# Kernel tuning notes

Hardware: AMD Instinct MI355X
Metric: run time of the kernel (lower is better)

The kernel has to match this reference:

```python
import jax, jax.numpy as jnp
import numpy as np

F, LP, NL, DG = 65536, 8, 8192, 64
D = 32  # path_state_dim == link_state_dim
ITERS = 8
MS = {'flow_traffic': (0.5, 2.0), 'flow_length': (0.5, 2.0), 'flow_loss_packet': (0.1, 5.0),
      'flow_propag_delay': (0.2, 3.0), 'link_capacity': (1.0, 1.0)}


def gru_cell(h, x, w, u, b):
    # Keras GRUCell (reset_after=True); gate order z, r, h
    mx = x @ w + b[0]
    mh = h @ u + b[1]
    xz, xr, xh = jnp.split(mx, 3, axis=-1)
    hz, hr, hh = jnp.split(mh, 3, axis=-1)
    z = jax.nn.sigmoid(xz + hz)
    r = jax.nn.sigmoid(xr + hr)
    c = jnp.tanh(xh + r * hh)
    return z * h + (1.0 - z) * c


def setup_inputs() -> dict:
    key = jax.random.key(0)
    ks = jax.random.split(key, 24)
    g = lambda i, shape: jax.random.normal(ks[i], shape, jnp.float32) * 0.1
    return dict(
        flow_traffic=jax.random.uniform(ks[0], (F, 1), jnp.float32),
        flow_length=jax.random.uniform(ks[1], (F, 1), jnp.float32),
        flow_loss_packet=jax.random.uniform(ks[2], (F, 1), jnp.float32),
        flow_propag_delay=jax.random.uniform(ks[3], (F, 1), jnp.float32),
        flow_packet_size=jax.random.uniform(ks[4], (F, 1), jnp.float32),
        link_capacity=jax.random.uniform(ks[5], (NL, 1), jnp.float32) + 0.5,
        link_to_flow=jax.random.randint(ks[6], (F, LP), 0, NL),
        flow_to_link_flow=jax.random.randint(ks[7], (NL, DG), 0, F),
        flow_to_link_pos=jax.random.randint(ks[8], (NL, DG), 0, LP + 1),
        fe_w1=g(9, (4, D)), fe_b1=jnp.zeros(D), fe_w2=g(10, (D, D)), fe_b2=jnp.zeros(D),
        le_w1=g(11, (2, D)), le_b1=jnp.zeros(D), le_w2=g(12, (D, D)), le_b2=jnp.zeros(D),
        att_w=g(13, (D, D)), att_b=jnp.zeros(D),
        pg_w=g(14, (D, 3 * D)), pg_u=g(15, (D, 3 * D)), pg_b=jnp.zeros((2, 3 * D)),
        lg_w=g(16, (D, 3 * D)), lg_u=g(17, (D, 3 * D)), lg_b=jnp.zeros((2, 3 * D)),
        ro_w1=g(18, (D, D // 2)), ro_b1=jnp.zeros(D // 2),
        ro_w2=g(19, (D // 2, D // 4)), ro_b2=jnp.zeros(D // 4),
        ro_w3=g(20, (D // 4, 1)), ro_b3=jnp.zeros(1),
    )


def reference(flow_traffic, flow_length, flow_loss_packet, flow_propag_delay, flow_packet_size,
              link_capacity, link_to_flow, flow_to_link_flow, flow_to_link_pos,
              fe_w1, fe_b1, fe_w2, fe_b2, le_w1, le_b1, le_w2, le_b2, att_w, att_b,
              pg_w, pg_u, pg_b, lg_w, lg_u, lg_b, ro_w1, ro_b1, ro_w2, ro_b2, ro_w3, ro_b3):
    norm = lambda x, k: (x - MS[k][0]) * MS[k][1]
    # per-link load: mean of traffic of flows crossing it / capacity  -> [NL,1]
    load = jnp.mean(flow_traffic[flow_to_link_flow], axis=1) / link_capacity
    pf = jnp.concatenate([norm(flow_traffic, 'flow_traffic'), norm(flow_length, 'flow_length'),
                          norm(flow_loss_packet, 'flow_loss_packet'),
                          norm(flow_propag_delay, 'flow_propag_delay')], axis=1)
    path_state = jax.nn.selu(jax.nn.selu(pf @ fe_w1 + fe_b1) @ fe_w2 + fe_b2)  # [F,D]
    lf = jnp.concatenate([norm(link_capacity, 'link_capacity'), load], axis=1)
    link_state = jax.nn.selu(jax.nn.selu(lf @ le_w1 + le_b1) @ le_w2 + le_b2)  # [NL,D]

    pss = None
    for _ in range(ITERS):
        link_gather = link_state[link_to_flow]  # [F,LP,D]
        prev = path_state

        def step(h, x):
            h2 = gru_cell(h, x, pg_w, pg_u, pg_b)
            return h2, h2

        path_state, seq = jax.lax.scan(step, prev, jnp.swapaxes(link_gather, 0, 1))
        seq = jnp.swapaxes(seq, 0, 1)  # [F,LP,D]
        pss = jnp.concatenate([prev[:, None, :], seq], axis=1)  # [F,LP+1,D]
        path_gather = pss[flow_to_link_flow, flow_to_link_pos]  # [NL,DG,D]
        attn = jax.nn.leaky_relu(path_gather @ att_w + att_b, negative_slope=0.2)
        score = jax.nn.softmax(attn, axis=-1)  # K.softmax default axis=-1
        agg = jnp.sum(score * path_gather, axis=1)  # [NL,D]
        link_state = gru_cell(link_state, agg, lg_w, lg_u, lg_b)

    h = jax.nn.selu(pss[:, 1:] @ ro_w1 + ro_b1)
    h = jax.nn.selu(h @ ro_w2 + ro_b2)
    occupancy = jax.nn.softplus(h @ ro_w3 + ro_b3)  # [F,LP,1]
    capacity_gather = link_capacity[link_to_flow]  # [F,LP,1]
    delay = jnp.sum(occupancy / capacity_gather, axis=1)  # [F,1]
    return delay + flow_propag_delay
```

## Files before the change

### kernel.cpp

```cpp
#include <hip/hip_runtime.h>
#include <hip/hip_bf16.h>
#include <cstddef>

#define F_    65536
#define LP_   8
#define NL_   8192
#define DG_   64
#define D_    32
#define ITERS_ 8

typedef short bf16x8 __attribute__((ext_vector_type(8)));
typedef float f32x2 __attribute__((ext_vector_type(2)));
typedef float f32x4 __attribute__((ext_vector_type(4)));
typedef float f32x16 __attribute__((ext_vector_type(16)));
typedef unsigned int u32x4 __attribute__((ext_vector_type(4)));

__device__ __forceinline__ float sigmoidf_(float x) { return 1.0f / (1.0f + __expf(-x)); }
__device__ __forceinline__ float tanhf_(float x)    { return 1.0f - 2.0f / (__expf(2.0f * x) + 1.0f); }
__device__ __forceinline__ float seluf_(float x) {
    const float a = 1.6732632423543772f, s = 1.0507009873554805f;
    return x > 0.0f ? s * x : s * a * (__expf(x) - 1.0f);
}
__device__ __forceinline__ float softplusf_(float x) { return x > 20.0f ? x : log1pf(__expf(x)); }

#define REP32(M) M(0)M(1)M(2)M(3)M(4)M(5)M(6)M(7)M(8)M(9)M(10)M(11)M(12)M(13)M(14)M(15) \
                 M(16)M(17)M(18)M(19)M(20)M(21)M(22)M(23)M(24)M(25)M(26)M(27)M(28)M(29)M(30)M(31)

#define BC32(src, i) __int_as_float(__builtin_amdgcn_ds_swizzle(__float_as_int(src), ((i) << 5)))

__device__ __forceinline__ unsigned int cvtpk_bf16(float a, float b) {
    unsigned int r;
    asm("v_cvt_pk_bf16_f32 %0, %1, %2" : "=v"(r) : "v"(a), "v"(b));
    return r;
}
__device__ __forceinline__ float bf_lo(unsigned int u) { return __uint_as_float(u << 16); }
__device__ __forceinline__ float bf_hi(unsigned int u) { return __uint_as_float(u & 0xFFFF0000u); }

__device__ __forceinline__ void mk_frag_w(f32x4 v0, f32x4 v1, u32x4& uh, u32x4& ul) {
    uh.x = cvtpk_bf16(v0.x, v0.y);
    uh.y = cvtpk_bf16(v0.z, v0.w);
    uh.z = cvtpk_bf16(v1.x, v1.y);
    uh.w = cvtpk_bf16(v1.z, v1.w);
    ul.x = cvtpk_bf16(v0.x - bf_lo(uh.x), v0.y - bf_hi(uh.x));
    ul.y = cvtpk_bf16(v0.z - bf_lo(uh.y), v0.w - bf_hi(uh.y));
    ul.z = cvtpk_bf16(v1.x - bf_lo(uh.z), v1.y - bf_hi(uh.z));
    ul.w = cvtpk_bf16(v1.z - bf_lo(uh.w), v1.w - bf_hi(uh.w));
}
__device__ __forceinline__ void mk_frag(f32x4 v0, f32x4 v1, bf16x8& hi, bf16x8& lo) {
    u32x4 uh, ul;
    mk_frag_w(v0, v1, uh, ul);
    hi = __builtin_bit_cast(bf16x8, uh);
    lo = __builtin_bit_cast(bf16x8, ul);
}

__global__ __launch_bounds__(256) void k_init_path(
    const float* __restrict__ tr, const float* __restrict__ len,
    const float* __restrict__ loss, const float* __restrict__ prop,
    const float* __restrict__ fe_w1, const float* __restrict__ fe_b1,
    const float* __restrict__ fe_w2, const float* __restrict__ fe_b2,
    float* __restrict__ h32)
{
    const int j = threadIdx.x & 31;
    const int half = (threadIdx.x >> 5) & 1;
    float w2c[32];
#pragma unroll
    for (int i = 0; i < 32; i++) w2c[i] = fe_w2[i * 32 + j];
    const float w10 = fe_w1[j], w11 = fe_w1[32 + j], w12 = fe_w1[64 + j], w13 = fe_w1[96 + j];
    const float b1 = fe_b1[j], b2 = fe_b2[j];
    const int wave = (blockIdx.x * blockDim.x + threadIdx.x) >> 6;
    const int nw = (gridDim.x * blockDim.x) >> 6;
    for (int fp = wave; fp < F_ / 2; fp += nw) {
        const int f = fp * 2 + half;
        float p0 = (tr[f]   - 0.5f) * 2.0f;
        float p1 = (len[f]  - 0.5f) * 2.0f;
        float p2 = (loss[f] - 0.1f) * 5.0f;
        float p3 = (prop[f] - 0.2f) * 3.0f;
        float h1 = seluf_(fmaf(p0, w10, fmaf(p1, w11, fmaf(p2, w12, fmaf(p3, w13, b1)))));
        float acc = b2;
#define ISTEP(i) { float hv = BC32(h1, i); acc = fmaf(hv, w2c[i], acc); }
        REP32(ISTEP)
#undef ISTEP
        h32[(size_t)f * 32 + j] = seluf_(acc);
    }
}

__global__ __launch_bounds__(256) void k_init_link(
    const float* __restrict__ tr, const float* __restrict__ cap, const int* __restrict__ f2lf,
    const float* __restrict__ le_w1, const float* __restrict__ le_b1,
    const float* __restrict__ le_w2, const float* __restrict__ le_b2,
    float* __restrict__ link_state, unsigned int* __restrict__ ls_pack)
{
    const int lane = threadIdx.x & 63;
    const int j = lane & 31;
    float w2c[32];
#pragma unroll
    for (int i = 0; i < 32; i++) w2c[i] = le_w2[i * 32 + j];
    const float w10 = le_w1[j], w11 = le_w1[32 + j];
    const float b1 = le_b1[j], b2 = le_b2[j];
    const int wave = (blockIdx.x * blockDim.x + threadIdx.x) >> 6;
    const int nw = (gridDim.x * blockDim.x) >> 6;
    for (int l = wave; l < NL_; l += nw) {
        int fidx = f2lf[l * 64 + lane];
        float s = tr[fidx];
        s += __shfl_xor(s, 1);  s += __shfl_xor(s, 2);  s += __shfl_xor(s, 4);
        s += __shfl_xor(s, 8);  s += __shfl_xor(s, 16); s += __shfl_xor(s, 32);
        float c = cap[l];
        float load = s * (1.0f / 64.0f) / c;
        float lf0 = (c - 1.0f);
        float h1 = seluf_(fmaf(lf0, w10, fmaf(load, w11, b1)));
        float acc = b2;
#define LSTEP(i) { float hv = BC32(h1, i); acc = fmaf(hv, w2c[i], acc); }
        REP32(LSTEP)
#undef LSTEP
        float lsv = seluf_(acc);
        float a = __shfl(lsv, 2 * (j & 15));
        float b = __shfl(lsv, 2 * (j & 15) + 1);
        unsigned int hw = cvtpk_bf16(a, b);
        unsigned int lw = cvtpk_bf16(a - bf_lo(hw), b - bf_hi(hw));
        if (lane < 32) {
            link_state[l * 32 + j] = lsv;
            ls_pack[l * 32 + j] = (j < 16) ? hw : lw;
        }
    }
}

__global__ __launch_bounds__(256, 3) void k_path(
    const unsigned int* __restrict__ ls_pack, const float* __restrict__ pg_u,
    const float* __restrict__ pg_w, const float* __restrict__ pg_b,
    const int* __restrict__ l2f,
    unsigned short* __restrict__ pss_bf, float* __restrict__ h32)
{
    __shared__ __align__(16) float xlds[4][576];
    __shared__ u32x4 wfrag[2][12][64];
    const int lane = threadIdx.x & 63;
    const int wid = threadIdx.x >> 6;
    const int jj = lane & 15;
    const int g4 = lane >> 4;
    const int task = (blockIdx.x * blockDim.x + threadIdx.x) >> 6;
    const int fb = task * 16;

    for (int tl = wid; tl < 12; tl += 4) {
        const float* base = (tl < 6) ? pg_u : pg_w;
        const int tc = (tl < 6) ? tl : tl - 6;
        const float* up = base + (g4 * 8) * 96 + tc * 16 + jj;
        f32x4 v0 = f32x4{up[0],   up[96],  up[192], up[288]};
        f32x4 v1 = f32x4{up[384], up[480], up[576], up[672]};
        u32x4 uh, ul;
        mk_frag_w(v0, v1, uh, ul);
        wfrag[0][tl][lane] = uh;
        wfrag[1][tl][lane] = ul;
    }
    __syncthreads();

    float b_z[2], b_r[2], b_0h[2], b_1h[2];
#pragma unroll
    for (int hf = 0; hf < 2; hf++) {
        const int idx = hf * 16 + jj;
        b_z[hf]  = pg_b[idx]      + pg_b[96 + idx];
        b_r[hf]  = pg_b[32 + idx] + pg_b[96 + 32 + idx];
        b_0h[hf] = pg_b[64 + idx];
        b_1h[hf] = pg_b[96 + 64 + idx];
    }
    unsigned short* pbase = pss_bf + (size_t)(fb + jj) * 288;
    float* hbase = h32 + (size_t)(fb + jj) * 32;
    f32x4 v0 = *(const f32x4*)(hbase + g4 * 8);
    f32x4 v1 = *(const f32x4*)(hbase + g4 * 8 + 4);
    bf16x8 ahi, alo;
    {
        u32x4 uh, ul;
        mk_frag_w(v0, v1, uh, ul);
        *(u32x4*)(pbase + g4 * 8) = uh;
        ahi = __builtin_bit_cast(bf16x8, uh);
        alo = __builtin_bit_cast(bf16x8, ul);
    }
    float hC[4][2];
#pragma unroll
    for (int r = 0; r < 4; r++) {
        const float* hp = h32 + (size_t)(fb + 4 * g4 + r) * 32;
        hC[r][0] = hp[jj];
        hC[r][1] = hp[jj + 16];
    }
    float* wl = &xlds[wid][0];

    int lks[8];
    {
        const int* lrow = l2f + (fb + jj) * 8;
#pragma unroll
        for (int t = 0; t < 8; t++) lks[t] = lrow[t];
    }
    const u32x4* lsp = (const u32x4*)ls_pack;
    u32x4 lsh_n = lsp[lks[0] * 8 + g4];
    u32x4 lsl_n = lsp[lks[0] * 8 + 4 + g4];

#pragma unroll
    for (int t = 0; t < 8; t++) {
        bf16x8 xhi = __builtin_bit_cast(bf16x8, lsh_n);
        bf16x8 xlo = __builtin_bit_cast(bf16x8, lsl_n);
        if (t < 7) {
            lsh_n = lsp[lks[t + 1] * 8 + g4];
            lsl_n = lsp[lks[t + 1] * 8 + 4 + g4];
        }
        f32x4 acc[8];
#pragma unroll
        for (int a = 0; a < 8; a++) acc[a] = f32x4{0.0f, 0.0f, 0.0f, 0.0f};
#pragma unroll
        for (int tl = 0; tl < 6; tl++) {
            int tlx = tl;
            asm volatile("" : "+v"(tlx));
            bf16x8 bh = __builtin_bit_cast(bf16x8, wfrag[0][tlx][lane]);
            bf16x8 bl = __builtin_bit_cast(bf16x8, wfrag[1][tlx][lane]);
            const int a = (tl < 4) ? tl : 4 + (tl & 1);
            acc[a] = __builtin_amdgcn_mfma_f32_16x16x32_bf16(ahi, bh, acc[a], 0, 0, 0);
            acc[a] = __builtin_amdgcn_mfma_f32_16x16x32_bf16(ahi, bl, acc[a], 0, 0, 0);
            acc[a] = __builtin_amdgcn_mfma_f32_16x16x32_bf16(alo, bh, acc[a], 0, 0, 0);
        }
#pragma unroll
        for (int tl = 0; tl < 6; tl++) {
            int tlx = 6 + tl;
            asm volatile("" : "+v"(tlx));
            bf16x8 bh = __builtin_bit_cast(bf16x8, wfrag[0][tlx][lane]);
            bf16x8 bl = __builtin_bit_cast(bf16x8, wfrag[1][tlx][lane]);
            const int a = (tl < 4) ? tl : 6 + (tl & 1);
            acc[a] = __builtin_amdgcn_mfma_f32_16x16x32_bf16(xhi, bh, acc[a], 0, 0, 0);
            acc[a] = __builtin_amdgcn_mfma_f32_16x16x32_bf16(xhi, bl, acc[a], 0, 0, 0);
            acc[a] = __builtin_amdgcn_mfma_f32_16x16x32_bf16(xlo, bh, acc[a], 0, 0, 0);
        }
#pragma unroll
        for (int r = 0; r < 4; r++) {
#pragma unroll
            for (int hf = 0; hf < 2; hf++) {
                float z  = sigmoidf_(acc[0 + hf][r] + b_z[hf]);
                float rg = sigmoidf_(acc[2 + hf][r] + b_r[hf]);
                float c  = tanhf_(acc[6 + hf][r] + b_0h[hf] + rg * (acc[4 + hf][r] + b_1h[hf]));
                float hn = fmaf(z, hC[r][hf] - c, c);
                hC[r][hf] = hn;
                wl[(4 * g4 + r) * 36 + jj + hf * 16] = hn;
            }
        }
        f32x4 n0 = *(const f32x4*)&wl[jj * 36 + g4 * 8];
        f32x4 n1 = *(const f32x4*)&wl[jj * 36 + g4 * 8 + 4];
        u32x4 uh, ul;
        mk_frag_w(n0, n1, uh, ul);
        *(u32x4*)(pbase + (t + 1) * 32 + g4 * 8) = uh;
        if (t < 7) {
            ahi = __builtin_bit_cast(bf16x8, uh);
            alo = __builtin_bit_cast(bf16x8, ul);
        } else {
            *(f32x4*)(hbase + g4 * 8)     = n0;
            *(f32x4*)(hbase + g4 * 8 + 4) = n1;
        }
    }
}

__global__ __launch_bounds__(256, 3) void k_att_fused(
    const unsigned short* __restrict__ pss_bf, const int* __restrict__ f2lf, const int* __restrict__ f2lp,
    const float* __restrict__ att_w, const float* __restrict__ att_b,
    const float* __restrict__ lg_w, const float* __restrict__ lg_u, const float* __restrict__ lg_b,
    float* __restrict__ link_state, unsigned int* __restrict__ ls_pack)
{
    __shared__ float xbuf[4][32];
    const int w = threadIdx.x >> 6;
    const int lane = threadIdx.x & 63;
    const int p31 = lane & 31;
    const int h = lane >> 5;
    const int l = blockIdx.x * 4 + w;
    const int j = p31;

    const int fi = f2lf[l * 64 + lane];
    const int pi = f2lp[l * 64 + lane];
    const unsigned int* rowp = (const unsigned int*)(pss_bf + ((size_t)fi * 9 + pi) * 32);
    u32x4 g0 = *(const u32x4*)(rowp + 0);
    u32x4 g1 = *(const u32x4*)(rowp + 4);
    u32x4 g2 = *(const u32x4*)(rowp + 8);
    u32x4 g3 = *(const u32x4*)(rowp + 12);
    unsigned int own[16] = {g0.x, g0.y, g0.z, g0.w, g1.x, g1.y, g1.z, g1.w,
                            g2.x, g2.y, g2.z, g2.w, g3.x, g3.y, g3.z, g3.w};
    unsigned int swp[16];
#pragma unroll
    for (int i = 0; i < 16; i++) swp[i] = __shfl_xor(own[i], 32);

    bf16x8 awhi[2], awlo[2];
#pragma unroll
    for (int kt = 0; kt < 2; kt++) {
        const float* wp = att_w + (kt * 16 + h * 8) * 32 + p31;
        f32x4 a0 = f32x4{wp[0],   wp[32],  wp[64],  wp[96]};
        f32x4 a1 = f32x4{wp[128], wp[160], wp[192], wp[224]};
        mk_frag(a0, a1, awhi[kt], awlo[kt]);
    }
    f32x4 ab[4];
#pragma unroll
    for (int rg = 0; rg < 4; rg++) {
        const float* bp = att_b + 8 * rg + 4 * h;
        ab[rg] = f32x4{bp[0], bp[1], bp[2], bp[3]};
    }

    bf16x8 B0[2], B1[2];
#pragma unroll
    for (int kt = 0; kt < 2; kt++) {
        u32x4 b0, b1;
#pragma unroll
        for (int e = 0; e < 4; e++) {
            unsigned int v0 = h ? swp[8 * kt + 4 + e] : own[8 * kt + e];
            unsigned int v1 = h ? own[8 * kt + 4 + e] : swp[8 * kt + e];
            ((unsigned int*)&b0)[e] = v0;
            ((unsigned int*)&b1)[e] = v1;
        }
        B0[kt] = __builtin_bit_cast(bf16x8, b0);
        B1[kt] = __builtin_bit_cast(bf16x8, b1);
    }

    f32x16 acc0{}, acc1{};
#pragma unroll
    for (int kt = 0; kt < 2; kt++) {
        acc0 = __builtin_amdgcn_mfma_f32_32x32x16_bf16(awhi[kt], B0[kt], acc0, 0, 0, 0);
        acc0 = __builtin_amdgcn_mfma_f32_32x32x16_bf16(awlo[kt], B0[kt], acc0, 0, 0, 0);
        acc1 = __builtin_amdgcn_mfma_f32_32x32x16_bf16(awhi[kt], B1[kt], acc1, 0, 0, 0);
        acc1 = __builtin_amdgcn_mfma_f32_32x32x16_bf16(awlo[kt], B1[kt], acc1, 0, 0, 0);
    }

    float q0[16], q1[16];
#pragma unroll
    for (int ph = 0; ph < 2; ph++) {
        float v[16];
#pragma unroll
        for (int r = 0; r < 16; r++) {
            float bias = ((const float*)&ab[r >> 2])[r & 3];
            float x = (ph == 0 ? acc0[r] : acc1[r]) + bias;
            v[r] = x > 0.0f ? x : 0.2f * x;
        }
        float m = v[0];
#pragma unroll
        for (int r = 1; r < 16; r++) m = fmaxf(m, v[r]);
        m = fmaxf(m, __shfl_xor(m, 32));
        float sm = 0.0f;
#pragma unroll
        for (int r = 0; r < 16; r++) { v[r] = __expf(v[r] - m); sm += v[r]; }
        sm += __shfl_xor(sm, 32);
        float inv = 1.0f / sm;
        float* q = (ph == 0) ? q0 : q1;
#pragma unroll
        for (int r = 0; r < 16; r++) {
            const int q4 = r >> 2, s = (r & 3) >> 1;
            unsigned int pv;
            if (ph == 0) pv = h ? swp[4 * q4 + 2 + s] : own[4 * q4 + s];
            else         pv = h ? own[4 * q4 + 2 + s] : swp[4 * q4 + s];
            float pf = (r & 1) ? bf_hi(pv) : bf_lo(pv);
            q[r] = v[r] * inv * pf;
        }
    }
    float qs[16];
#pragma unroll
    for (int r = 0; r < 16; r++) qs[r] = q0[r] + q1[r];
#pragma unroll
    for (int d = 1; d < 32; d <<= 1) {
#pragma unroll
        for (int r = 0; r < 16; r++) qs[r] += __shfl_xor(qs[r], d);
    }
    if (p31 == 0) {
#pragma unroll
        for (int r = 0; r < 16; r++) xbuf[w][(r & 3) + 8 * (r >> 2) + 4 * h] = qs[r];
    }
    float s = xbuf[w][j];

    const float hval = link_state[l * 32 + j];
    float src = (lane < 32) ? hval : s;
    const float* wb = (lane < 32) ? lg_u : lg_w;
    float p0 = (lane < 32) ? lg_b[96 + j]      : lg_b[j];
    float p1 = (lane < 32) ? lg_b[96 + 32 + j] : lg_b[32 + j];
    float p2 = (lane < 32) ? lg_b[96 + 64 + j] : lg_b[64 + j];
#define ASTEP(i) { float vv = BC32(src, i); \
    p0 = fmaf(vv, wb[(i) * 96 + j], p0); \
    p1 = fmaf(vv, wb[(i) * 96 + 32 + j], p1); \
    p2 = fmaf(vv, wb[(i) * 96 + 64 + j], p2); }
    REP32(ASTEP)
#undef ASTEP
    float t0 = __shfl_xor(p0, 32);
    float t1 = __shfl_xor(p1, 32);
    float t2 = __shfl_xor(p2, 32);
    float hn = 0.0f;
    if (lane < 32) {
        float z = sigmoidf_(t0 + p0);
        float r = sigmoidf_(t1 + p1);
        float c = tanhf_(t2 + r * p2);
        hn = fmaf(z, hval, (1.0f - z) * c);
        link_state[l * 32 + j] = hn;
    }
    float a = __shfl(hn, 2 * (j & 15));
    float b = __shfl(hn, 2 * (j & 15) + 1);
    unsigned int hw = cvtpk_bf16(a, b);
    unsigned int lw = cvtpk_bf16(a - bf_lo(hw), b - bf_hi(hw));
    if (lane < 32) ls_pack[l * 32 + j] = (j < 16) ? hw : lw;
}

__global__ __launch_bounds__(256) void k_readout(
    const unsigned short* __restrict__ pss_bf, const int* __restrict__ l2f,
    const float* __restrict__ cap, const float* __restrict__ prop,
    const float* __restrict__ ro_w1, const float* __restrict__ b1,
    const float* __restrict__ ro_w2, const float* __restrict__ b2,
    const float* __restrict__ w3, const float* __restrict__ b3,
    float* __restrict__ out)
{
    const int tid = blockIdx.x * blockDim.x + threadIdx.x;
    const int f = tid >> 3, t = tid & 7;
    const unsigned int* rowp = (const unsigned int*)(pss_bf + ((size_t)f * 9 + 1 + t) * 32);
    float xr[32];
#pragma unroll
    for (int i = 0; i < 4; i++) {
        u32x4 v = *(const u32x4*)(rowp + 4 * i);
        xr[8 * i + 0] = bf_lo(v.x); xr[8 * i + 1] = bf_hi(v.x);
        xr[8 * i + 2] = bf_lo(v.y); xr[8 * i + 3] = bf_hi(v.y);
        xr[8 * i + 4] = bf_lo(v.z); xr[8 * i + 5] = bf_hi(v.z);
        xr[8 * i + 6] = bf_lo(v.w); xr[8 * i + 7] = bf_hi(v.w);
    }
    float h1[16];
#pragma unroll
    for (int jj = 0; jj < 16; jj++) {
        float acc = b1[jj];
#pragma unroll
        for (int i = 0; i < 32; i++) acc = fmaf(xr[i], ro_w1[i * 16 + jj], acc);
        h1[jj] = seluf_(acc);
    }
    float h2[8];
#pragma unroll
    for (int jj = 0; jj < 8; jj++) {
        float acc = b2[jj];
#pragma unroll
        for (int i = 0; i < 16; i++) acc = fmaf(h1[i], ro_w2[i * 8 + jj], acc);
        h2[jj] = seluf_(acc);
    }
    float o = b3[0];
#pragma unroll
    for (int i = 0; i < 8; i++) o = fmaf(h2[i], w3[i], o);
    o = softplusf_(o);
    int link = l2f[f * 8 + t];
    float v = o / cap[link];
    v += __shfl_xor(v, 1, 8);
    v += __shfl_xor(v, 2, 8);
    v += __shfl_xor(v, 4, 8);
    if (t == 0) out[f] = v + prop[f];
}

extern "C" void kernel_launch(void* const* d_in, const int* in_sizes, int n_in,
                              void* d_out, int out_size, void* d_ws, size_t ws_size,
                              hipStream_t stream) {
    const float* flow_traffic = (const float*)d_in[0];
    const float* flow_length  = (const float*)d_in[1];
    const float* flow_loss    = (const float*)d_in[2];
    const float* flow_prop    = (const float*)d_in[3];
    const float* link_cap     = (const float*)d_in[5];
    const int*   l2f          = (const int*)d_in[6];
    const int*   f2lf         = (const int*)d_in[7];
    const int*   f2lp         = (const int*)d_in[8];
    const float* fe_w1 = (const float*)d_in[9],  *fe_b1 = (const float*)d_in[10];
    const float* fe_w2 = (const float*)d_in[11], *fe_b2 = (const float*)d_in[12];
    const float* le_w1 = (const float*)d_in[13], *le_b1 = (const float*)d_in[14];
    const float* le_w2 = (const float*)d_in[15], *le_b2 = (const float*)d_in[16];
    const float* att_w = (const float*)d_in[17], *att_b = (const float*)d_in[18];
    const float* pg_w  = (const float*)d_in[19], *pg_u  = (const float*)d_in[20], *pg_b = (const float*)d_in[21];
    const float* lg_w  = (const float*)d_in[22], *lg_u  = (const float*)d_in[23], *lg_b = (const float*)d_in[24];
    const float* ro_w1 = (const float*)d_in[25], *ro_b1 = (const float*)d_in[26];
    const float* ro_w2 = (const float*)d_in[27], *ro_b2 = (const float*)d_in[28];
    const float* ro_w3 = (const float*)d_in[29], *ro_b3 = (const float*)d_in[30];
    float* out = (float*)d_out;

    unsigned short* pss_bf = (unsigned short*)d_ws;
    float* h32        = (float*)(pss_bf + (size_t)F_ * 288);
    float* link_state = h32 + (size_t)F_ * 32;
    unsigned int* ls_pack = (unsigned int*)(link_state + NL_ * 32);

    k_init_path<<<512, 256, 0, stream>>>(flow_traffic, flow_length, flow_loss, flow_prop,
                                         fe_w1, fe_b1, fe_w2, fe_b2, h32);
    k_init_link<<<512, 256, 0, stream>>>(flow_traffic, link_cap, f2lf,
                                         le_w1, le_b1, le_w2, le_b2, link_state, ls_pack);
    for (int it = 0; it < ITERS_; ++it) {
        k_path<<<F_ / 64, 256, 0, stream>>>(ls_pack, pg_u, pg_w, pg_b, l2f, pss_bf, h32);
        k_att_fused<<<NL_ / 4, 256, 0, stream>>>(pss_bf, f2lf, f2lp, att_w, att_b,
                                                 lg_w, lg_u, lg_b, link_state, ls_pack);
    }
    k_readout<<<F_ * 8 / 256, 256, 0, stream>>>(pss_bf, l2f, link_cap, flow_prop,
                                                ro_w1, ro_b1, ro_w2, ro_b2, ro_w3, ro_b3, out);
}
```

Measured before the change: 560.3 us.

## Permute path-state feature layout to drop LDS transpose in path GRU

Path state is stored in a permuted feature order so that the MFMA output layout of the path GRU directly matches the layout needed for the next step's input fragment. The per-step LDS write/read transpose and its buffer are removed, and operand roles in the MFMAs are swapped (weights as A, state as B). Consumers (init, attention weights, readout) are adjusted to the permuted order. This trades LDS traffic and bank contention for more index bookkeeping, and a mistake in any permutation would break correctness.

Result: no change. 564.4 us (+0.7%).

```diff
diff --git a/kernel.cpp b/kernel.cpp
--- a/kernel.cpp
+++ b/kernel.cpp
@@ -14,6 +14,7 @@
 typedef float f32x4 __attribute__((ext_vector_type(4)));
 typedef float f32x16 __attribute__((ext_vector_type(16)));
 typedef unsigned int u32x4 __attribute__((ext_vector_type(4)));
+
 
 __device__ __forceinline__ float sigmoidf_(float x) { return 1.0f / (1.0f + __expf(-x)); }
 __device__ __forceinline__ float tanhf_(float x)    { return 1.0f - 2.0f / (__expf(2.0f * x) + 1.0f); }
@@ -67,6 +68,7 @@
     for (int i = 0; i < 32; i++) w2c[i] = fe_w2[i * 32 + j];
     const float w10 = fe_w1[j], w11 = fe_w1[32 + j], w12 = fe_w1[64 + j], w13 = fe_w1[96 + j];
     const float b1 = fe_b1[j], b2 = fe_b2[j];
+    const int pj = 8 * ((j >> 2) & 3) + 2 * (j & 3) + (j >> 4);
     const int wave = (blockIdx.x * blockDim.x + threadIdx.x) >> 6;
     const int nw = (gridDim.x * blockDim.x) >> 6;
     for (int fp = wave; fp < F_ / 2; fp += nw) {
@@ -80,7 +82,7 @@
 #define ISTEP(i) { float hv = BC32(h1, i); acc = fmaf(hv, w2c[i], acc); }
         REP32(ISTEP)
 #undef ISTEP
-        h32[(size_t)f * 32 + j] = seluf_(acc);
+        h32[(size_t)f * 32 + pj] = seluf_(acc);
     }
 }
 
@@ -130,76 +132,75 @@
     const int* __restrict__ l2f,
     unsigned short* __restrict__ pss_bf, float* __restrict__ h32)
 {
-    __shared__ __align__(16) float xlds[4][576];
     __shared__ u32x4 wfrag[2][12][64];
     const int lane = threadIdx.x & 63;
-    const int wid = threadIdx.x >> 6;
-    const int jj = lane & 15;
-    const int g4 = lane >> 4;
+    const int wid  = threadIdx.x >> 6;
+    const int jj   = lane & 15;
+    const int g    = lane >> 4;
     const int task = (blockIdx.x * blockDim.x + threadIdx.x) >> 6;
-    const int fb = task * 16;
+    const int fme  = task * 16 + jj;
 
     for (int tl = wid; tl < 12; tl += 4) {
-        const float* base = (tl < 6) ? pg_u : pg_w;
-        const int tc = (tl < 6) ? tl : tl - 6;
-        const float* up = base + (g4 * 8) * 96 + tc * 16 + jj;
-        f32x4 v0 = f32x4{up[0],   up[96],  up[192], up[288]};
-        f32x4 v1 = f32x4{up[384], up[480], up[576], up[672]};
+        float v[8];
+        if (tl < 6) {
+#pragma unroll
+            for (int e = 0; e < 8; e++) {
+                const int d = 4 * g + (e >> 1) + 16 * (e & 1);
+                v[e] = pg_u[d * 96 + tl * 16 + jj];
+            }
+        } else {
+#pragma unroll
+            for (int e = 0; e < 8; e++)
+                v[e] = pg_w[(8 * g + e) * 96 + (tl - 6) * 16 + jj];
+        }
         u32x4 uh, ul;
-        mk_frag_w(v0, v1, uh, ul);
+        mk_frag_w(f32x4{v[0], v[1], v[2], v[3]}, f32x4{v[4], v[5], v[6], v[7]}, uh, ul);
         wfrag[0][tl][lane] = uh;
         wfrag[1][tl][lane] = ul;
     }
     __syncthreads();
 
-    float b_z[2], b_r[2], b_0h[2], b_1h[2];
-#pragma unroll
-    for (int hf = 0; hf < 2; hf++) {
-        const int idx = hf * 16 + jj;
-        b_z[hf]  = pg_b[idx]      + pg_b[96 + idx];
-        b_r[hf]  = pg_b[32 + idx] + pg_b[96 + 32 + idx];
-        b_0h[hf] = pg_b[64 + idx];
-        b_1h[hf] = pg_b[96 + 64 + idx];
-    }
-    unsigned short* pbase = pss_bf + (size_t)(fb + jj) * 288;
-    float* hbase = h32 + (size_t)(fb + jj) * 32;
-    f32x4 v0 = *(const f32x4*)(hbase + g4 * 8);
-    f32x4 v1 = *(const f32x4*)(hbase + g4 * 8 + 4);
-    bf16x8 ahi, alo;
-    {
-        u32x4 uh, ul;
-        mk_frag_w(v0, v1, uh, ul);
-        *(u32x4*)(pbase + g4 * 8) = uh;
-        ahi = __builtin_bit_cast(bf16x8, uh);
-        alo = __builtin_bit_cast(bf16x8, ul);
-    }
-    float hC[4][2];
-#pragma unroll
-    for (int r = 0; r < 4; r++) {
-        const float* hp = h32 + (size_t)(fb + 4 * g4 + r) * 32;
-        hC[r][0] = hp[jj];
-        hC[r][1] = hp[jj + 16];
-    }
-    float* wl = &xlds[wid][0];
+    float b_z[4][2], b_r[4][2], b0h[4][2], b1h[4][2];
+#pragma unroll
+    for (int r = 0; r < 4; r++)
+#pragma unroll
+        for (int hf = 0; hf < 2; hf++) {
+            const int d = 16 * hf + 4 * g + r;
+            b_z[r][hf] = pg_b[d]      + pg_b[96 + d];
+            b_r[r][hf] = pg_b[32 + d] + pg_b[96 + 32 + d];
+            b0h[r][hf] = pg_b[64 + d];
+            b1h[r][hf] = pg_b[96 + 64 + d];
+        }
+
+    unsigned short* pbase = pss_bf + (size_t)fme * 288;
+    float* hbase = h32 + (size_t)fme * 32;
+    f32x4 v0 = *(const f32x4*)(hbase + 8 * g);
+    f32x4 v1 = *(const f32x4*)(hbase + 8 * g + 4);
+    u32x4 bhw, blw;
+    mk_frag_w(v0, v1, bhw, blw);
+    *(u32x4*)(pbase + 8 * g) = bhw;
+    float hC[4][2] = {{v0.x, v0.y}, {v0.z, v0.w}, {v1.x, v1.y}, {v1.z, v1.w}};
 
     int lks[8];
     {
-        const int* lrow = l2f + (fb + jj) * 8;
+        const int* lrow = l2f + fme * 8;
 #pragma unroll
         for (int t = 0; t < 8; t++) lks[t] = lrow[t];
     }
     const u32x4* lsp = (const u32x4*)ls_pack;
-    u32x4 lsh_n = lsp[lks[0] * 8 + g4];
-    u32x4 lsl_n = lsp[lks[0] * 8 + 4 + g4];
+    u32x4 lsh_n = lsp[lks[0] * 8 + g];
+    u32x4 lsl_n = lsp[lks[0] * 8 + 4 + g];
 
 #pragma unroll
     for (int t = 0; t < 8; t++) {
         bf16x8 xhi = __builtin_bit_cast(bf16x8, lsh_n);
         bf16x8 xlo = __builtin_bit_cast(bf16x8, lsl_n);
         if (t < 7) {
-            lsh_n = lsp[lks[t + 1] * 8 + g4];
-            lsl_n = lsp[lks[t + 1] * 8 + 4 + g4];
-        }
+            lsh_n = lsp[lks[t + 1] * 8 + g];
+            lsl_n = lsp[lks[t + 1] * 8 + 4 + g];
+        }
+        bf16x8 hhi = __builtin_bit_cast(bf16x8, bhw);
+        bf16x8 hlo = __builtin_bit_cast(bf16x8, blw);
         f32x4 acc[8];
 #pragma unroll
         for (int a = 0; a < 8; a++) acc[a] = f32x4{0.0f, 0.0f, 0.0f, 0.0f};
@@ -207,47 +208,45 @@
         for (int tl = 0; tl < 6; tl++) {
             int tlx = tl;
             asm volatile("" : "+v"(tlx));
-            bf16x8 bh = __builtin_bit_cast(bf16x8, wfrag[0][tlx][lane]);
-            bf16x8 bl = __builtin_bit_cast(bf16x8, wfrag[1][tlx][lane]);
+            bf16x8 ah = __builtin_bit_cast(bf16x8, wfrag[0][tlx][lane]);
+            bf16x8 al = __builtin_bit_cast(bf16x8, wfrag[1][tlx][lane]);
             const int a = (tl < 4) ? tl : 4 + (tl & 1);
-            acc[a] = __builtin_amdgcn_mfma_f32_16x16x32_bf16(ahi, bh, acc[a], 0, 0, 0);
-            acc[a] = __builtin_amdgcn_mfma_f32_16x16x32_bf16(ahi, bl, acc[a], 0, 0, 0);
-            acc[a] = __builtin_amdgcn_mfma_f32_16x16x32_bf16(alo, bh, acc[a], 0, 0, 0);
+            acc[a] = __builtin_amdgcn_mfma_f32_16x16x32_bf16(ah, hhi, acc[a], 0, 0, 0);
+            acc[a] = __builtin_amdgcn_mfma_f32_16x16x32_bf16(al, hhi, acc[a], 0, 0, 0);
+            acc[a] = __builtin_amdgcn_mfma_f32_16x16x32_bf16(ah, hlo, acc[a], 0, 0, 0);
         }
 #pragma unroll
         for (int tl = 0; tl < 6; tl++) {
             int tlx = 6 + tl;
             asm volatile("" : "+v"(tlx));
-            bf16x8 bh = __builtin_bit_cast(bf16x8, wfrag[0][tlx][lane]);
-            bf16x8 bl = __builtin_bit_cast(bf16x8, wfrag[1][tlx][lane]);
+            bf16x8 ah = __builtin_bit_cast(bf16x8, wfrag[0][tlx][lane]);
+            bf16x8 al = __builtin_bit_cast(bf16x8, wfrag[1][tlx][lane]);
             const int a = (tl < 4) ? tl : 6 + (tl & 1);
-            acc[a] = __builtin_amdgcn_mfma_f32_16x16x32_bf16(xhi, bh, acc[a], 0, 0, 0);
-            acc[a] = __builtin_amdgcn_mfma_f32_16x16x32_bf16(xhi, bl, acc[a], 0, 0, 0);
-            acc[a] = __builtin_amdgcn_mfma_f32_16x16x32_bf16(xlo, bh, acc[a], 0, 0, 0);
-        }
-#pragma unroll
-        for (int r = 0; r < 4; r++) {
+            acc[a] = __builtin_amdgcn_mfma_f32_16x16x32_bf16(ah, xhi, acc[a], 0, 0, 0);
+            acc[a] = __builtin_amdgcn_mfma_f32_16x16x32_bf16(al, xhi, acc[a], 0, 0, 0);
+            acc[a] = __builtin_amdgcn_mfma_f32_16x16x32_bf16(ah, xlo, acc[a], 0, 0, 0);
+        }
+#pragma unroll
+        for (int r = 0; r < 4; r++)
 #pragma unroll
             for (int hf = 0; hf < 2; hf++) {
-                float z  = sigmoidf_(acc[0 + hf][r] + b_z[hf]);
-                float rg = sigmoidf_(acc[2 + hf][r] + b_r[hf]);
-                float c  = tanhf_(acc[6 + hf][r] + b_0h[hf] + rg * (acc[4 + hf][r] + b_1h[hf]));
-                float hn = fmaf(z, hC[r][hf] - c, c);
-                hC[r][hf] = hn;
-                wl[(4 * g4 + r) * 36 + jj + hf * 16] = hn;
+                float z  = sigmoidf_(acc[0 + hf][r] + b_z[r][hf]);
+                float rg = sigmoidf_(acc[2 + hf][r] + b_r[r][hf]);
+                float c  = tanhf_(acc[6 + hf][r] + b0h[r][hf] + rg * (acc[4 + hf][r] + b1h[r][hf]));
+                hC[r][hf] = fmaf(z, hC[r][hf] - c, c);
             }
-        }
-        f32x4 n0 = *(const f32x4*)&wl[jj * 36 + g4 * 8];
-        f32x4 n1 = *(const f32x4*)&wl[jj * 36 + g4 * 8 + 4];
-        u32x4 uh, ul;
-        mk_frag_w(n0, n1, uh, ul);
-        *(u32x4*)(pbase + (t + 1) * 32 + g4 * 8) = uh;
-        if (t < 7) {
-            ahi = __builtin_bit_cast(bf16x8, uh);
-            alo = __builtin_bit_cast(bf16x8, ul);
-        } else {
-            *(f32x4*)(hbase + g4 * 8)     = n0;
-            *(f32x4*)(hbase + g4 * 8 + 4) = n1;
+        bhw.x = cvtpk_bf16(hC[0][0], hC[0][1]);
+        bhw.y = cvtpk_bf16(hC[1][0], hC[1][1]);
+        bhw.z = cvtpk_bf16(hC[2][0], hC[2][1]);
+        bhw.w = cvtpk_bf16(hC[3][0], hC[3][1]);
+        blw.x = cvtpk_bf16(hC[0][0] - bf_lo(bhw.x), hC[0][1] - bf_hi(bhw.x));
+        blw.y = cvtpk_bf16(hC[1][0] - bf_lo(bhw.y), hC[1][1] - bf_hi(bhw.y));
+        blw.z = cvtpk_bf16(hC[2][0] - bf_lo(bhw.z), hC[2][1] - bf_hi(bhw.z));
+        blw.w = cvtpk_bf16(hC[3][0] - bf_lo(bhw.w), hC[3][1] - bf_hi(bhw.w));
+        *(u32x4*)(pbase + (t + 1) * 32 + 8 * g) = bhw;
+        if (t == 7) {
+            *(f32x4*)(hbase + 8 * g)     = f32x4{hC[0][0], hC[0][1], hC[1][0], hC[1][1]};
+            *(f32x4*)(hbase + 8 * g + 4) = f32x4{hC[2][0], hC[2][1], hC[3][0], hC[3][1]};
         }
     }
 }
@@ -282,9 +281,11 @@
     bf16x8 awhi[2], awlo[2];
 #pragma unroll
     for (int kt = 0; kt < 2; kt++) {
-        const float* wp = att_w + (kt * 16 + h * 8) * 32 + p31;
-        f32x4 a0 = f32x4{wp[0],   wp[32],  wp[64],  wp[96]};
-        f32x4 a1 = f32x4{wp[128], wp[160], wp[192], wp[224]};
+        const int B4 = 4 * (2 * kt + h);
+        f32x4 a0 = f32x4{att_w[(B4 + 0) * 32 + p31], att_w[(B4 + 16) * 32 + p31],
+                         att_w[(B4 + 1) * 32 + p31], att_w[(B4 + 17) * 32 + p31]};
+        f32x4 a1 = f32x4{att_w[(B4 + 2) * 32 + p31], att_w[(B4 + 18) * 32 + p31],
+                         att_w[(B4 + 3) * 32 + p31], att_w[(B4 + 19) * 32 + p31]};
         mk_frag(a0, a1, awhi[kt], awlo[kt]);
     }
     f32x4 ab[4];
@@ -340,11 +341,13 @@
         float* q = (ph == 0) ? q0 : q1;
 #pragma unroll
         for (int r = 0; r < 16; r++) {
-            const int q4 = r >> 2, s = (r & 3) >> 1;
+            const int q4 = r >> 2, rl = r & 3;
+            const int wA = 8 * (q4 & 1) + rl;
+            const int wB = 8 * (q4 & 1) + 4 + rl;
             unsigned int pv;
-            if (ph == 0) pv = h ? swp[4 * q4 + 2 + s] : own[4 * q4 + s];
-            else         pv = h ? own[4 * q4 + 2 + s] : swp[4 * q4 + s];
-            float pf = (r & 1) ? bf_hi(pv) : bf_lo(pv);
+            if (ph == 0) pv = h ? swp[wB] : own[wA];
+            else         pv = h ? own[wB] : swp[wA];
+            float pf = (q4 & 2) ? bf_hi(pv) : bf_lo(pv);
             q[r] = v[r] * inv * pf;
         }
     }
@@ -417,7 +420,10 @@
     for (int jj = 0; jj < 16; jj++) {
         float acc = b1[jj];
 #pragma unroll
-        for (int i = 0; i < 32; i++) acc = fmaf(xr[i], ro_w1[i * 16 + jj], acc);
+        for (int p = 0; p < 32; p++) {
+            const int d = 4 * (p >> 3) + ((p & 7) >> 1) + 16 * (p & 1);
+            acc = fmaf(xr[p], ro_w1[d * 16 + jj], acc);
+        }
         h1[jj] = seluf_(acc);
     }
     float h2[8];
```
